# Optimization experiments

Measured on AMD Instinct MI355X. Metric: run time of the kernel, lower is better.

The kernel has to match this reference:

```python
import jax, jax.numpy as jnp
import numpy as np


def setup_inputs() -> dict:
    key = jax.random.key(0)
    ks = jax.random.split(key, 6)
    B, L, R, A, D = 256, 196, 1024, 512, 2048
    return {
        "h": jax.random.normal(ks[0], (B, R), dtype=jnp.float32),
        "att_feats1": jax.random.normal(ks[1], (B, L, D), dtype=jnp.float32),
        "att_feats2": jax.random.normal(ks[2], (B, L, A), dtype=jnp.float32),
        "att_masks": jnp.ones((B, L), dtype=jnp.float32),
        "W_h": jax.random.normal(ks[3], (R, A), dtype=jnp.float32) * (1.0 / np.sqrt(R)),
        "b_h": jnp.zeros((A,), dtype=jnp.float32),
        "w_a": jax.random.normal(ks[4], (A,), dtype=jnp.float32) * (1.0 / np.sqrt(A)),
        "b_a": jnp.zeros((), dtype=jnp.float32),
    }


def reference(h, att_feats1, att_feats2, att_masks, W_h, b_h, w_a, b_a):
    # att_h = h2att(h): [B, A]
    att_h = h @ W_h + b_h
    # dot = alpha_net(tanh(att_feats2 + att_h[:, None, :])): [B, L]
    dot = jnp.einsum("bla,a->bl", jnp.tanh(att_feats2 + att_h[:, None, :]), w_a) + b_a
    weight = jax.nn.softmax(dot, axis=1)  # [B, L]
    # masked renormalization
    weight = weight * att_masks
    weight = weight / jnp.sum(weight, axis=1, keepdims=True)
    # weighted sum over regions: [B, D]
    att = jnp.einsum("bl,bld->bd", weight, att_feats1)
    return att
```

## Files before the change

kernel.cpp:

```cpp
#include <hip/hip_runtime.h>

#define BB 256
#define LL 196
#define RR 1024
#define AA 512
#define DD 2048

__device__ __forceinline__ float fast_tanh(float x) {
    float e = __expf(2.0f * x);
    float r = __builtin_amdgcn_rcpf(e + 1.0f);
    return 1.0f - 2.0f * r;
}

__global__ __launch_bounds__(256) void gemm_hWh(const float* __restrict__ h,
                                                const float* __restrict__ W,
                                                const float* __restrict__ bh,
                                                float* __restrict__ out) {
    __shared__ float As[32][33];
    __shared__ float Bs[32][33];
    const int bn = blockIdx.x;
    const int bm = blockIdx.y;
    const int t  = threadIdx.x;
    const int ty = t >> 4, tx = t & 15;
    const int lr = t >> 3;
    const int lc = (t & 7) * 4;

    float acc00 = 0.f, acc01 = 0.f, acc10 = 0.f, acc11 = 0.f;

    for (int k0 = 0; k0 < RR; k0 += 32) {
        float4 a4 = *(const float4*)&h[(size_t)(bm * 32 + lr) * RR + k0 + lc];
        float4 b4 = *(const float4*)&W[(size_t)(k0 + lr) * AA + bn * 32 + lc];
        As[lr][lc + 0] = a4.x; As[lr][lc + 1] = a4.y;
        As[lr][lc + 2] = a4.z; As[lr][lc + 3] = a4.w;
        Bs[lr][lc + 0] = b4.x; Bs[lr][lc + 1] = b4.y;
        Bs[lr][lc + 2] = b4.z; Bs[lr][lc + 3] = b4.w;
        __syncthreads();
#pragma unroll
        for (int kk = 0; kk < 32; ++kk) {
            float a0 = As[ty * 2 + 0][kk];
            float a1 = As[ty * 2 + 1][kk];
            float b0 = Bs[kk][tx * 2 + 0];
            float b1 = Bs[kk][tx * 2 + 1];
            acc00 += a0 * b0; acc01 += a0 * b1;
            acc10 += a1 * b0; acc11 += a1 * b1;
        }
        __syncthreads();
    }
    const int gm = bm * 32 + ty * 2;
    const int gn = bn * 32 + tx * 2;
    out[(size_t)(gm + 0) * AA + gn + 0] = acc00 + bh[gn + 0];
    out[(size_t)(gm + 0) * AA + gn + 1] = acc01 + bh[gn + 1];
    out[(size_t)(gm + 1) * AA + gn + 0] = acc10 + bh[gn + 0];
    out[(size_t)(gm + 1) * AA + gn + 1] = acc11 + bh[gn + 1];
}

__global__ __launch_bounds__(256) void attn_weights(
    const float* __restrict__ f2,
    const float* __restrict__ masks,
    const float* __restrict__ att_h,
    const float* __restrict__ w_a,
    const float* __restrict__ b_a,
    float* __restrict__ weight)
{
    __shared__ float ah[AA];
    __shared__ float wa[AA];
    __shared__ float dot[LL];
    __shared__ float red[256];

    const int b = blockIdx.x;
    const int t = threadIdx.x;

    for (int i = t; i < AA; i += 256) {
        ah[i] = att_h[(size_t)b * AA + i];
        wa[i] = w_a[i];
    }
    __syncthreads();

    const int wave = t >> 6, lane = t & 63;
    const float ba = b_a[0];
    const float* f2b = f2 + (size_t)b * LL * AA;

    for (int l = wave; l < LL; l += 4) {
        const float4* row = (const float4*)(f2b + (size_t)l * AA);
        const float4* ah4 = (const float4*)ah;
        const float4* wa4 = (const float4*)wa;
        float partial = 0.f;
#pragma unroll
        for (int j = 0; j < 2; ++j) {
            int idx = lane + 64 * j;
            float4 v = row[idx];
            float4 av = ah4[idx];
            float4 wv = wa4[idx];
            partial += fast_tanh(v.x + av.x) * wv.x;
            partial += fast_tanh(v.y + av.y) * wv.y;
            partial += fast_tanh(v.z + av.z) * wv.z;
            partial += fast_tanh(v.w + av.w) * wv.w;
        }
#pragma unroll
        for (int off = 32; off; off >>= 1) partial += __shfl_down(partial, off);
        if (lane == 0) dot[l] = partial + ba;
    }
    __syncthreads();

    float v = (t < LL) ? dot[t] : -1e30f;
    red[t] = v;
    __syncthreads();
#pragma unroll
    for (int s = 128; s; s >>= 1) {
        if (t < s) red[t] = fmaxf(red[t], red[t + s]);
        __syncthreads();
    }
    const float m = red[0];
    __syncthreads();
    float e = 0.f;
    if (t < LL) e = __expf(dot[t] - m) * masks[(size_t)b * LL + t];
    red[t] = e;
    __syncthreads();
#pragma unroll
    for (int s = 128; s; s >>= 1) {
        if (t < s) red[t] += red[t + s];
        __syncthreads();
    }
    const float inv = 1.0f / red[0];
    if (t < LL) weight[(size_t)b * LL + t] = e * inv;
}

__global__ __launch_bounds__(256) void weighted_sum(
    const float* __restrict__ f1,
    const float* __restrict__ weight,
    float* __restrict__ out)
{
    __shared__ float w[LL];
    const int b = blockIdx.y;
    const int t = threadIdx.x;
    const int d0 = blockIdx.x * 1024 + t * 4;

    if (t < LL) w[t] = weight[(size_t)b * LL + t];
    __syncthreads();

    const float* base = f1 + (size_t)b * LL * DD + d0;
    float4 acc = {0.f, 0.f, 0.f, 0.f};
#pragma unroll 4
    for (int l = 0; l < LL; ++l) {
        float4 v = *(const float4*)(base + (size_t)l * DD);
        float wl = w[l];
        acc.x += wl * v.x; acc.y += wl * v.y;
        acc.z += wl * v.z; acc.w += wl * v.w;
    }
    *(float4*)&out[(size_t)b * DD + d0] = acc;
}

extern "C" void kernel_launch(void* const* d_in, const int* in_sizes, int n_in,
                              void* d_out, int out_size, void* d_ws, size_t ws_size,
                              hipStream_t stream) {
    const float* h   = (const float*)d_in[0];
    const float* f1  = (const float*)d_in[1];
    const float* f2  = (const float*)d_in[2];
    const float* msk = (const float*)d_in[3];
    const float* W   = (const float*)d_in[4];
    const float* bh  = (const float*)d_in[5];
    const float* wa  = (const float*)d_in[6];
    const float* ba  = (const float*)d_in[7];
    float* out = (float*)d_out;

    float* att_h  = (float*)d_ws;
    float* weight = att_h + (size_t)BB * AA;

    gemm_hWh<<<dim3(16, 8), 256, 0, stream>>>(h, W, bh, att_h);
    attn_weights<<<BB, 256, 0, stream>>>(f2, msk, att_h, wa, ba, weight);
    weighted_sum<<<dim3(2, BB), 256, 0, stream>>>(f1, weight, out);
}
```

Baseline: 650.7 us.

## Fuse attention weights and weighted sum into one 1024-thread kernel

Merges the softmax-weight kernel and the weighted-sum kernel into a single kernel with 1024 threads per batch, keeping weights in shared memory instead of a global round-trip. Score computation uses 16 waves with att_h/w_a held in registers, and the D reduction splits L in two halves combined through shared memory. The b_a bias is dropped, since softmax is shift-invariant. Risk: only 256 blocks of 1024 threads, so occupancy and memory-level parallelism for the f1 stream may be lower than the previous 512-block grid.

Measured after the change: 634.3 us. -2.5%, faster.

```diff
diff --git a/kernel.cpp b/kernel.cpp
--- a/kernel.cpp
+++ b/kernel.cpp
@@ -8,8 +8,7 @@
 
 __device__ __forceinline__ float fast_tanh(float x) {
     float e = __expf(2.0f * x);
-    float r = __builtin_amdgcn_rcpf(e + 1.0f);
-    return 1.0f - 2.0f * r;
+    return 1.0f - 2.0f * __builtin_amdgcn_rcpf(e + 1.0f);
 }
 
 __global__ __launch_bounds__(256) void gemm_hWh(const float* __restrict__ h,
@@ -54,56 +53,48 @@
     out[(size_t)(gm + 1) * AA + gn + 1] = acc11 + bh[gn + 1];
 }
 
-__global__ __launch_bounds__(256) void attn_weights(
+__global__ __launch_bounds__(1024) void attn_fused(
+    const float* __restrict__ f1,
     const float* __restrict__ f2,
     const float* __restrict__ masks,
     const float* __restrict__ att_h,
     const float* __restrict__ w_a,
-    const float* __restrict__ b_a,
-    float* __restrict__ weight)
+    float* __restrict__ out)
 {
-    __shared__ float ah[AA];
-    __shared__ float wa[AA];
     __shared__ float dot[LL];
     __shared__ float red[256];
+    __shared__ float w[LL];
+    __shared__ float sacc[512 * 4];
 
     const int b = blockIdx.x;
     const int t = threadIdx.x;
+    const int wave = t >> 6, lane = t & 63;
 
-    for (int i = t; i < AA; i += 256) {
-        ah[i] = att_h[(size_t)b * AA + i];
-        wa[i] = w_a[i];
+    const float4* ah4 = (const float4*)(att_h + (size_t)b * AA);
+    const float4* wa4 = (const float4*)w_a;
+    const float4 a0 = ah4[lane * 2], a1 = ah4[lane * 2 + 1];
+    const float4 w0 = wa4[lane * 2], w1 = wa4[lane * 2 + 1];
+
+    const float4* f2b = (const float4*)(f2 + (size_t)b * LL * AA);
+
+    for (int l = wave; l < LL; l += 16) {
+        float4 v0 = f2b[l * 128 + lane * 2];
+        float4 v1 = f2b[l * 128 + lane * 2 + 1];
+        float p = fast_tanh(v0.x + a0.x) * w0.x
+                + fast_tanh(v0.y + a0.y) * w0.y
+                + fast_tanh(v0.z + a0.z) * w0.z
+                + fast_tanh(v0.w + a0.w) * w0.w
+                + fast_tanh(v1.x + a1.x) * w1.x
+                + fast_tanh(v1.y + a1.y) * w1.y
+                + fast_tanh(v1.z + a1.z) * w1.z
+                + fast_tanh(v1.w + a1.w) * w1.w;
+#pragma unroll
+        for (int off = 32; off; off >>= 1) p += __shfl_down(p, off);
+        if (lane == 0) dot[l] = p;
     }
     __syncthreads();
 
-    const int wave = t >> 6, lane = t & 63;
-    const float ba = b_a[0];
-    const float* f2b = f2 + (size_t)b * LL * AA;
-
-    for (int l = wave; l < LL; l += 4) {
-        const float4* row = (const float4*)(f2b + (size_t)l * AA);
-        const float4* ah4 = (const float4*)ah;
-        const float4* wa4 = (const float4*)wa;
-        float partial = 0.f;
-#pragma unroll
-        for (int j = 0; j < 2; ++j) {
-            int idx = lane + 64 * j;
-            float4 v = row[idx];
-            float4 av = ah4[idx];
-            float4 wv = wa4[idx];
-            partial += fast_tanh(v.x + av.x) * wv.x;
-            partial += fast_tanh(v.y + av.y) * wv.y;
-            partial += fast_tanh(v.z + av.z) * wv.z;
-            partial += fast_tanh(v.w + av.w) * wv.w;
-        }
-#pragma unroll
-        for (int off = 32; off; off >>= 1) partial += __shfl_down(partial, off);
-        if (lane == 0) dot[l] = partial + ba;
-    }
-    __syncthreads();
-
-    float v = (t < LL) ? dot[t] : -1e30f;
-    red[t] = v;
+    if (t < 256) red[t] = (t < LL) ? dot[t] : -1e30f;
     __syncthreads();
 #pragma unroll
     for (int s = 128; s; s >>= 1) {
@@ -114,40 +105,36 @@
     __syncthreads();
     float e = 0.f;
     if (t < LL) e = __expf(dot[t] - m) * masks[(size_t)b * LL + t];
-    red[t] = e;
+    if (t < 256) red[t] = e;
     __syncthreads();
 #pragma unroll
     for (int s = 128; s; s >>= 1) {
         if (t < s) red[t] += red[t + s];
         __syncthreads();
     }
-    const float inv = 1.0f / red[0];
-    if (t < LL) weight[(size_t)b * LL + t] = e * inv;
-}
-
-__global__ __launch_bounds__(256) void weighted_sum(
-    const float* __restrict__ f1,
-    const float* __restrict__ weight,
-    float* __restrict__ out)
-{
-    __shared__ float w[LL];
-    const int b = blockIdx.y;
-    const int t = threadIdx.x;
-    const int d0 = blockIdx.x * 1024 + t * 4;
-
-    if (t < LL) w[t] = weight[(size_t)b * LL + t];
+    if (t < LL) w[t] = e * (1.0f / red[0]);
     __syncthreads();
 
-    const float* base = f1 + (size_t)b * LL * DD + d0;
+    const int u    = t & 511;
+    const int half = t >> 9;
+    const float4* f1b = (const float4*)(f1 + (size_t)b * LL * DD) + u;
     float4 acc = {0.f, 0.f, 0.f, 0.f};
-#pragma unroll 4
-    for (int l = 0; l < LL; ++l) {
-        float4 v = *(const float4*)(base + (size_t)l * DD);
-        float wl = w[l];
+    const int l0 = half * 98;
+#pragma unroll 7
+    for (int i = 0; i < 98; ++i) {
+        const int l = l0 + i;
+        float4 v = f1b[(size_t)l * 512];
+        const float wl = w[l];
         acc.x += wl * v.x; acc.y += wl * v.y;
         acc.z += wl * v.z; acc.w += wl * v.w;
     }
-    *(float4*)&out[(size_t)b * DD + d0] = acc;
+    if (half == 1) *(float4*)&sacc[u * 4] = acc;
+    __syncthreads();
+    if (half == 0) {
+        float4 o = *(float4*)&sacc[u * 4];
+        acc.x += o.x; acc.y += o.y; acc.z += o.z; acc.w += o.w;
+        *(float4*)&out[(size_t)b * DD + u * 4] = acc;
+    }
 }
 
 extern "C" void kernel_launch(void* const* d_in, const int* in_sizes, int n_in,
@@ -160,13 +147,10 @@
     const float* W   = (const float*)d_in[4];
     const float* bh  = (const float*)d_in[5];
     const float* wa  = (const float*)d_in[6];
-    const float* ba  = (const float*)d_in[7];
     float* out = (float*)d_out;
 
-    float* att_h  = (float*)d_ws;
-    float* weight = att_h + (size_t)BB * AA;
+    float* att_h = (float*)d_ws;
 
     gemm_hWh<<<dim3(16, 8), 256, 0, stream>>>(h, W, bh, att_h);
-    attn_weights<<<BB, 256, 0, stream>>>(f2, msk, att_h, wa, ba, weight);
-    weighted_sum<<<dim3(2, BB), 256, 0, stream>>>(f1, weight, out);
+    attn_fused<<<BB, 1024, 0, stream>>>(f1, f2, msk, att_h, wa, out);
 }
```
